# Kernel tuning notes

Measured on AMD Instinct MI355X. Metric: run time of the kernel, lower is better.

The kernel has to match this reference:

```python
import jax, jax.numpy as jnp
import numpy as np

BETA = 0.25  # commitment_beta


def setup_inputs() -> dict:
    key = jax.random.key(0)
    k1, k2 = jax.random.split(key)
    x = jax.random.normal(k1, (16, 256, 32, 32), dtype=jnp.float32)
    # codebook weight: (n_embed + 1, embed_dim); last row is the padding idx (zeros)
    weight = jax.random.normal(k2, (8193, 256), dtype=jnp.float32) * 0.05
    weight = weight.at[-1].set(0.0)
    return {"x": x, "weight": weight}


def reference(x, weight):
    # Eval-mode forward of VectorQuantize2 (accept_image_fmap=True, no EMA update).
    B, C, H, W = x.shape
    xf = jnp.transpose(x, (0, 2, 3, 1)).reshape(B, H * W, C)  # b (h w) c
    emb = weight[:-1]  # [N, C], drop padding row
    # squared euclidean distance; argmin identical to torch.cdist argmin
    d2 = (
        jnp.sum(xf * xf, axis=-1, keepdims=True)
        - 2.0 * jnp.einsum("bnc,kc->bnk", xf, emb)
        + jnp.sum(emb * emb, axis=-1)
    )  # [B, HW, N]
    code = jnp.argmin(d2, axis=-1)  # [B, HW]
    x_q = emb[code]  # [B, HW, C]
    loss = BETA * jnp.mean((jax.lax.stop_gradient(x_q) - xf) ** 2) + jnp.mean(
        (x_q - jax.lax.stop_gradient(xf)) ** 2
    )
    # straight-through estimator
    xq_st = xf + jax.lax.stop_gradient(x_q - xf)
    xq_out = jnp.transpose(xq_st.reshape(B, H, W, C), (0, 3, 1, 2))  # b c h w
    code_out = code.reshape(B, H, W)
    return xq_out, loss, code_out
```

## Files before the change

### kernel.cpp

```cpp
#include <hip/hip_runtime.h>
#include <hip/hip_bf16.h>


#define N_ROWS   16384
#define KCODES   8192
#define DIM      256
#define LOSS_OFF 4194304
#define CODE_OFF 4194305
#define MARGIN_ACC 0.006f

typedef _Float16 half8  __attribute__((ext_vector_type(8)));
typedef _Float16 half4v __attribute__((ext_vector_type(4)));
typedef float    float4v __attribute__((ext_vector_type(4)));
typedef float    float2v __attribute__((ext_vector_type(2)));
typedef unsigned long long u64;

__device__ __forceinline__ unsigned umax32(unsigned a, unsigned b) { return a > b ? a : b; }
__device__ __forceinline__ unsigned umin32(unsigned a, unsigned b) { return a < b ? a : b; }
__device__ __forceinline__ void gll16(const _Float16* g, _Float16* l) {
  __builtin_amdgcn_global_load_lds((const __attribute__((address_space(1))) void*)g,
                                   (__attribute__((address_space(3))) void*)l, 16, 0, 0);
}


__global__ __launch_bounds__(256) void k_prep(const float* __restrict__ x, _Float16* __restrict__ xh,
                                              const float* __restrict__ wt, _Float16* __restrict__ eh,
                                              float* __restrict__ en2c, float* __restrict__ sxxp,
                                              double* __restrict__ dacc, unsigned* __restrict__ cnt) {
  __shared__ float lsx[128 * 65];
  __shared__ __align__(16) _Float16 ls[8192];
  __shared__ float es[32];
  int t = threadIdx.x;
  int lane = t & 63, wv = t >> 6;
  int bid = blockIdx.x;
  if (bid < 512) {
    if (bid == 0 && t == 0) { dacc[0] = 0.0; *cnt = 0u; }
    int blk = bid >> 2, cc = bid & 3;
    int row0 = blk * 128;
    int b    = row0 >> 10;
    int n0   = row0 & 1023;
    const float* xb = x + (size_t)b * 262144 + n0;
    int c_off = t >> 6;
    int nn    = (t & 63) * 2;
    float sxx = 0.f;
    for (int j = 0; j < 16; ++j) {
      int c = cc * 64 + j * 4 + c_off;
      float2v v = *(const float2v*)&xb[(size_t)c * 1024 + nn];
      int cp = c & 63;
      sxx = fmaf(v[0], v[0], sxx);
      sxx = fmaf(v[1], v[1], sxx);
      lsx[nn * 65 + cp]       = v[0];
      lsx[(nn + 1) * 65 + cp] = v[1];
    }
    __syncthreads();
#pragma unroll
    for (int i = 0; i < 4; ++i) {
      int unit = i * 256 + t;
      int rl = unit >> 3, p = unit & 7;
      const float* src = &lsx[rl * 65 + p * 8];
      half8 h;
#pragma unroll
      for (int k2 = 0; k2 < 8; ++k2) h[k2] = (_Float16)src[k2];
      int p7 = p ^ (rl & 7);
      *(half8*)&xh[(size_t)blk * 32768 + (size_t)cc * 8192 + (size_t)rl * 64 + p7 * 8] = h;
    }
#pragma unroll
    for (int d = 32; d; d >>= 1) sxx += __shfl_xor(sxx, d);
    __syncthreads();
    if (lane == 0) lsx[wv] = sxx;
    __syncthreads();
    if (t == 0) sxxp[bid] = lsx[0] + lsx[1] + lsx[2] + lsx[3];
  } else {
    int blk  = bid - 512;
    int k0 = blk * 32;
    const float* wb = wt + (size_t)k0 * 256;
    for (int i = 0; i < 8; ++i) {
      int lin = i * 1024 + t * 4;
      float4v v = *(const float4v*)&wb[lin];
      half4v h; float ss = 0.f;
#pragma unroll
      for (int j = 0; j < 4; ++j) { h[j] = (_Float16)v[j]; ss = fmaf(v[j], v[j], ss); }
      *(half4v*)&ls[lin] = h;
#pragma unroll
      for (int d = 32; d; d >>= 1) ss += __shfl_xor(ss, d);
      if (lane == 0) es[i * 4 + wv] = ss;
    }
    __syncthreads();
    size_t tb = (size_t)(k0 >> 7) * 32768;
    for (int i = 0; i < 4; ++i) {
      int u = i * 256 + t;
      int code_l = u >> 5;
      int cu = u & 31, chunk = cu >> 3, p = cu & 7;
      int kgl = k0 + code_l;
      int kg = p ^ (kgl & 7);
      half8 h = *(half8*)&ls[code_l * 256 + chunk * 64 + kg * 8];
      *(half8*)&eh[tb + (size_t)chunk * 8192 + (size_t)(kgl & 127) * 64 + p * 8] = h;
    }
    if (t < 32) en2c[k0 + t] = 32.0f - 0.5f * es[t];
  }
}

__global__ __launch_bounds__(256) void k_gemm(const _Float16* __restrict__ xh, const _Float16* __restrict__ eh,
                                              const float* __restrict__ en2c,
                                              u64* __restrict__ top2) {
  __shared__ __align__(16) _Float16 As[8192];
  __shared__ __align__(16) _Float16 Bs[8192];
  int t    = threadIdx.x;
  int bx   = blockIdx.x;
  int by   = blockIdx.y;
  int lane = t & 63, w = t >> 6;
  int wr = w & 1, wc = w >> 1;
  int ln15 = lane & 15, q = lane >> 4;
  int q4 = q * 4;

  const _Float16* Ag = eh + (size_t)bx * 32768;
  const _Float16* Bg = xh + (size_t)by * 32768;

  int kwave = bx * 128 + wr * 64;
  float4v cin[4];
#pragma unroll
  for (int mi = 0; mi < 4; ++mi) cin[mi] = *(const float4v*)&en2c[kwave + mi * 16 + q4];

  float4v acc[4][4];
#pragma unroll
  for (int mi = 0; mi < 4; ++mi)
#pragma unroll
    for (int ni = 0; ni < 4; ++ni) acc[mi][ni] = cin[mi];

  int so = (w * 64 + lane) * 8;
  int lo = w * 512;

  for (int ch = 0; ch < 4; ++ch) {
    if (ch) __syncthreads();
    const _Float16* ac = Ag + ch * 8192;
    const _Float16* bc = Bg + ch * 8192;
#pragma unroll
    for (int i = 0; i < 4; ++i) {
      gll16(ac + i * 2048 + so, As + i * 2048 + lo);
      gll16(bc + i * 2048 + so, Bs + i * 2048 + lo);
    }
    __syncthreads();
#pragma unroll
    for (int ks = 0; ks < 2; ++ks) {
      half8 af[4], bf[4];
#pragma unroll
      for (int mi = 0; mi < 4; ++mi) {
        int row = wr * 64 + mi * 16 + ln15;
        af[mi] = *(const half8*)&As[(row * 8 + ((ks * 4 + q) ^ (row & 7))) * 8];
      }
#pragma unroll
      for (int ni = 0; ni < 4; ++ni) {
        int row = wc * 64 + ni * 16 + ln15;
        bf[ni] = *(const half8*)&Bs[(row * 8 + ((ks * 4 + q) ^ (row & 7))) * 8];
      }
#pragma unroll
      for (int mi = 0; mi < 4; ++mi)
#pragma unroll
        for (int ni = 0; ni < 4; ++ni)
          acc[mi][ni] = __builtin_amdgcn_mfma_f32_16x16x32_f16(af[mi], bf[ni], acc[mi][ni], 0, 0, 0);
    }
  }

  __syncthreads();
  u64* ep = (u64*)(void*)As;
  int ibase = wr * 64 + q4;

#pragma unroll
  for (int ni = 0; ni < 4; ++ni) {
    unsigned hi[8], lo2[8];
#pragma unroll
    for (int j = 0; j < 8; ++j) {
      int mi = j >> 1, rb = (j & 1) * 2;
      unsigned p0 = (__float_as_uint(acc[mi][ni][rb])     & 0xFFFFFF80u) | (unsigned)(ibase + mi * 16 + rb);
      unsigned p1 = (__float_as_uint(acc[mi][ni][rb + 1]) & 0xFFFFFF80u) | (unsigned)(ibase + mi * 16 + rb + 1);
      hi[j] = umax32(p0, p1); lo2[j] = umin32(p0, p1);
    }
#pragma unroll
    for (int st = 4; st; st >>= 1)
#pragma unroll
      for (int j = 0; j < 8; ++j) if (j < st) {
        unsigned nb = umax32(hi[j], hi[j + st]);
        unsigned ns = umax32(umin32(hi[j], hi[j + st]), umax32(lo2[j], lo2[j + st]));
        hi[j] = nb; lo2[j] = ns;
      }
    unsigned b = hi[0], s = lo2[0];
#pragma unroll
    for (int d = 16; d < 64; d <<= 1) {
      unsigned ob = __shfl_xor(b, d);
      unsigned os = __shfl_xor(s, d);
      unsigned ns = umax32(umin32(b, ob), umax32(s, os));
      b = umax32(b, ob); s = ns;
    }
    if (q == 0) {
      int rl = wc * 64 + ni * 16 + ln15;
      ep[rl * 2 + wr] = ((u64)b << 32) | s;
    }
  }
  __syncthreads();
  if (t < 128) {
    u64 A = ep[t * 2 + 0], B = ep[t * 2 + 1];
    unsigned a0 = (unsigned)(A >> 32), a1 = (unsigned)A;
    unsigned b0 = (unsigned)(B >> 32), b1 = (unsigned)B;
    unsigned best = umax32(a0, b0);
    unsigned sec  = umax32(umin32(a0, b0), umax32(a1, b1));
    top2[(size_t)bx * 16384 + (size_t)by * 128 + t] = ((u64)best << 32) | sec;
  }
}

__global__ __launch_bounds__(1024) void k_out(const u64* __restrict__ top2,
                                              const float* __restrict__ x, const float* __restrict__ w,
                                              float* __restrict__ out, const float* __restrict__ sxxp,
                                              double* __restrict__ dacc, unsigned* __restrict__ cnt) {
  __shared__ float ect[256 * 65];
  __shared__ double dpart[16];
  __shared__ unsigned oldc;
  int t    = threadIdx.x;
  int lane = t & 63, wv = t >> 6;
  int blk  = blockIdx.x;
  int row0 = blk * 64;
  int b = row0 >> 10, n0 = row0 & 1023;

  double dsum = 0.0;
  for (int j = 0; j < 4; ++j) {
    int rl  = wv * 4 + j;
    int row = row0 + rl;
    u64 e = top2[(size_t)lane * 16384 + row];
    unsigned hi = (unsigned)(e >> 32), lo = (unsigned)e;
    unsigned mx = hi;
#pragma unroll
    for (int d = 1; d < 64; d <<= 1) mx = umax32(mx, __shfl_xor(mx, d));
    float fm = __uint_as_float(mx & 0xFFFFFF80u);
    float th = fm - MARGIN_ACC;
    bool c0 = __uint_as_float(hi & 0xFFFFFF80u) >= th;
    bool c1 = __uint_as_float(lo & 0xFFFFFF80u) >= th;
    u64 bal0 = __ballot(c0), bal1 = __ballot(c1);
    int kbest;
    double d2c;
    if (__popcll(bal0) + __popcll(bal1) <= 1) {
      int l0 = __ffsll((unsigned long long)__ballot(hi == mx)) - 1;
      kbest = l0 * 128 + (int)(__shfl(hi, l0) & 127u);
      d2c = 64.0 - 2.0 * (double)fm;
    } else {
      const float* xr = x + (size_t)b * 262144 + (row & 1023);
      float4v ex;
#pragma unroll
      for (int i = 0; i < 4; ++i) ex[i] = xr[(size_t)(lane * 4 + i) * 1024];
      double bs = 1e300; int bk = 0x7fffffff;
      for (int pass = 0; pass < 2; ++pass) {
        u64 bal = pass ? bal1 : bal0;
        unsigned src = pass ? lo : hi;
        while (bal) {
          int l = __ffsll((unsigned long long)bal) - 1;
          bal &= bal - 1;
          int kc = l * 128 + (int)(__shfl(src, l) & 127u);
          float4v wv4 = *(const float4v*)&w[(size_t)kc * DIM + lane * 4];
          double s = 0.0;
#pragma unroll
          for (int i = 0; i < 4; ++i) { double ev = (double)wv4[i]; s += ev * (ev - 2.0 * (double)ex[i]); }
#pragma unroll
          for (int d = 1; d < 64; d <<= 1) s += __shfl_xor(s, d);
          if (s < bs || (s == bs && kc < bk)) { bs = s; bk = kc; }
        }
      }
      kbest = bk;
      d2c = bs;
    }
    if (lane == 0) { out[CODE_OFF + row] = (float)kbest; dsum += d2c; }
    const float* wrow = w + (size_t)kbest * 256;
#pragma unroll
    for (int i = 0; i < 4; ++i) ect[(i * 64 + lane) * 65 + rl] = wrow[i * 64 + lane];
  }
  __syncthreads();

  const size_t base = (size_t)b * 262144 + n0 + lane;
  for (int j = 0; j < 16; ++j) {
    int c = wv * 16 + j;
    out[base + (size_t)c * 1024] = ect[c * 65 + lane];
  }
  if (lane == 0) dpart[wv] = dsum;
  __syncthreads();
  if (t == 0) {
    double s = 0.0;
#pragma unroll
    for (int i = 0; i < 16; ++i) s += dpart[i];
    atomicAdd(&dacc[0], s);
    __threadfence();
    oldc = atomicAdd(cnt, 1u);
  }
  __syncthreads();
  if (oldc == 255u && t < 64) {
    float ps = 0.f;
#pragma unroll
    for (int i = 0; i < 8; ++i) ps += sxxp[t * 8 + i];
#pragma unroll
    for (int d = 32; d; d >>= 1) ps += __shfl_xor(ps, d);
    if (t == 0) {
      __threadfence();
      double sd2 = *(volatile double*)&dacc[0];
      out[LOSS_OFF] = (float)(1.25 * ((double)ps + sd2) / 4194304.0);
    }
  }
}

extern "C" void kernel_launch(void* const* d_in, const int* in_sizes, int n_in,
                              void* d_out, int out_size, void* d_ws, size_t ws_size,
                              hipStream_t stream) {
  const float* x = (const float*)d_in[0];
  const float* w = (const float*)d_in[1];
  float* out = (float*)d_out;
  char* ws = (char*)d_ws;
  _Float16* xh   = (_Float16*)(ws);
  _Float16* eh   = (_Float16*)(ws + 8388608);
  float*    en2c = (float*)(ws + 12582912);
  u64*      top2 = (u64*)(ws + 12615680);
  float*    sxxp = (float*)(ws + 21004288);
  double*   dacc = (double*)(ws + 21006336);
  unsigned* cnt  = (unsigned*)(ws + 21006344);

  k_prep<<<768, 256, 0, stream>>>(x, xh, w, eh, en2c, sxxp, dacc, cnt);
  k_gemm<<<dim3(64, 128), 256, 0, stream>>>(xh, eh, en2c, top2);
  k_out<<<256, 1024, 0, stream>>>(top2, x, w, out, sxxp, dacc, cnt);
}
```

Before: 174.7 us.

## Pipeline GEMM K-loop with 4-stage LDS ring and 32-wide K chunks

Changes the fp16 packed layout of x and codebook to 32-element K chunks with a 2-bit swizzle. The GEMM kernel now streams eight smaller chunks through a 4-slot LDS ring, prefetching two chunks ahead and using explicit vmcnt waits instead of a full load then barrier per chunk. MFMA blocks run at raised wave priority. The goal is to hide global-to-LDS latency behind compute, at the cost of more barriers and a dedicated epilogue buffer that adds LDS use.

```diff
diff --git a/kernel.cpp b/kernel.cpp
--- a/kernel.cpp
+++ b/kernel.cpp
@@ -56,13 +56,14 @@
 #pragma unroll
     for (int i = 0; i < 4; ++i) {
       int unit = i * 256 + t;
-      int rl = unit >> 3, p = unit & 7;
-      const float* src = &lsx[rl * 65 + p * 8];
+      int rl = unit >> 3, pp = unit & 7;
+      int chl = pp >> 2, kgp = pp & 3;
+      int kg  = kgp ^ ((rl >> 1) & 3);
+      const float* src = &lsx[rl * 65 + chl * 32 + kg * 8];
       half8 h;
 #pragma unroll
       for (int k2 = 0; k2 < 8; ++k2) h[k2] = (_Float16)src[k2];
-      int p7 = p ^ (rl & 7);
-      *(half8*)&xh[(size_t)blk * 32768 + (size_t)cc * 8192 + (size_t)rl * 64 + p7 * 8] = h;
+      *(half8*)&xh[(size_t)blk * 32768 + (size_t)(cc * 2 + chl) * 4096 + (size_t)rl * 32 + kgp * 8] = h;
     }
 #pragma unroll
     for (int d = 32; d; d >>= 1) sxx += __shfl_xor(sxx, d);
@@ -90,11 +91,11 @@
     for (int i = 0; i < 4; ++i) {
       int u = i * 256 + t;
       int code_l = u >> 5;
-      int cu = u & 31, chunk = cu >> 3, p = cu & 7;
-      int kgl = k0 + code_l;
-      int kg = p ^ (kgl & 7);
-      half8 h = *(half8*)&ls[code_l * 256 + chunk * 64 + kg * 8];
-      *(half8*)&eh[tb + (size_t)chunk * 8192 + (size_t)(kgl & 127) * 64 + p * 8] = h;
+      int cu = u & 31, ch = cu >> 2, kgp = cu & 3;
+      int rl = (k0 + code_l) & 127;
+      int kg = kgp ^ ((rl >> 1) & 3);
+      half8 h = *(half8*)&ls[code_l * 256 + ch * 32 + kg * 8];
+      *(half8*)&eh[tb + (size_t)ch * 4096 + (size_t)rl * 32 + kgp * 8] = h;
     }
     if (t < 32) en2c[k0 + t] = 32.0f - 0.5f * es[t];
   }
@@ -103,8 +104,9 @@
 __global__ __launch_bounds__(256) void k_gemm(const _Float16* __restrict__ xh, const _Float16* __restrict__ eh,
                                               const float* __restrict__ en2c,
                                               u64* __restrict__ top2) {
-  __shared__ __align__(16) _Float16 As[8192];
-  __shared__ __align__(16) _Float16 Bs[8192];
+  __shared__ __align__(16) _Float16 As[4][4096];
+  __shared__ __align__(16) _Float16 Bs[4][4096];
+  __shared__ u64 ep[256];
   int t    = threadIdx.x;
   int bx   = blockIdx.x;
   int by   = blockIdx.y;
@@ -127,42 +129,48 @@
 #pragma unroll
     for (int ni = 0; ni < 4; ++ni) acc[mi][ni] = cin[mi];
 
-  int so = (w * 64 + lane) * 8;
-  int lo = w * 512;
-
-  for (int ch = 0; ch < 4; ++ch) {
-    if (ch) __syncthreads();
-    const _Float16* ac = Ag + ch * 8192;
-    const _Float16* bc = Bg + ch * 8192;
-#pragma unroll
-    for (int i = 0; i < 4; ++i) {
-      gll16(ac + i * 2048 + so, As + i * 2048 + lo);
-      gll16(bc + i * 2048 + so, Bs + i * 2048 + lo);
-    }
-    __syncthreads();
-#pragma unroll
-    for (int ks = 0; ks < 2; ++ks) {
-      half8 af[4], bf[4];
-#pragma unroll
-      for (int mi = 0; mi < 4; ++mi) {
-        int row = wr * 64 + mi * 16 + ln15;
-        af[mi] = *(const half8*)&As[(row * 8 + ((ks * 4 + q) ^ (row & 7))) * 8];
-      }
-#pragma unroll
-      for (int ni = 0; ni < 4; ++ni) {
-        int row = wc * 64 + ni * 16 + ln15;
-        bf[ni] = *(const half8*)&Bs[(row * 8 + ((ks * 4 + q) ^ (row & 7))) * 8];
-      }
-#pragma unroll
-      for (int mi = 0; mi < 4; ++mi)
-#pragma unroll
-        for (int ni = 0; ni < 4; ++ni)
-          acc[mi][ni] = __builtin_amdgcn_mfma_f32_16x16x32_f16(af[mi], bf[ni], acc[mi][ni], 0, 0, 0);
-    }
-  }
-
-  __syncthreads();
-  u64* ep = (u64*)(void*)As;
+#pragma unroll
+  for (int c0 = 0; c0 < 2; ++c0) {
+    int off = c0 * 4096;
+    gll16(Ag + off + t * 8,        &As[c0][0]    + w * 512);
+    gll16(Ag + off + 2048 + t * 8, &As[c0][2048] + w * 512);
+    gll16(Bg + off + t * 8,        &Bs[c0][0]    + w * 512);
+    gll16(Bg + off + 2048 + t * 8, &Bs[c0][2048] + w * 512);
+  }
+
+#pragma unroll
+  for (int ch = 0; ch < 8; ++ch) {
+    if (ch < 7) asm volatile("s_waitcnt vmcnt(4)" ::: "memory");
+    else        asm volatile("s_waitcnt vmcnt(0)" ::: "memory");
+    __builtin_amdgcn_s_barrier();
+    __builtin_amdgcn_sched_barrier(0);
+    if (ch < 6) {
+      int off = (ch + 2) * 4096;
+      _Float16* An = &As[(ch + 2) & 3][0];
+      _Float16* Bn = &Bs[(ch + 2) & 3][0];
+      gll16(Ag + off + t * 8,        An        + w * 512);
+      gll16(Ag + off + 2048 + t * 8, An + 2048 + w * 512);
+      gll16(Bg + off + t * 8,        Bn        + w * 512);
+      gll16(Bg + off + 2048 + t * 8, Bn + 2048 + w * 512);
+    }
+    half8 af[4], bf[4];
+#pragma unroll
+    for (int mi = 0; mi < 4; ++mi) {
+      int rl = wr * 64 + mi * 16 + ln15;
+      af[mi] = *(const half8*)&As[ch & 3][rl * 32 + ((q ^ ((rl >> 1) & 3)) * 8)];
+      int rb = wc * 64 + mi * 16 + ln15;
+      bf[mi] = *(const half8*)&Bs[ch & 3][rb * 32 + ((q ^ ((rb >> 1) & 3)) * 8)];
+    }
+    __builtin_amdgcn_s_setprio(1);
+#pragma unroll
+    for (int mi = 0; mi < 4; ++mi)
+#pragma unroll
+      for (int ni = 0; ni < 4; ++ni)
+        acc[mi][ni] = __builtin_amdgcn_mfma_f32_16x16x32_f16(af[mi], bf[ni], acc[mi][ni], 0, 0, 0);
+    __builtin_amdgcn_s_setprio(0);
+  }
+
+  __syncthreads();
   int ibase = wr * 64 + q4;
 
 #pragma unroll
```

Measured after the change: 183.5 us. 1.05x slower.
